# Optimization experiments

Measured on AMD Instinct MI355X. Metric: run time of the kernel, lower is better.

## Reference

```python
import jax, jax.numpy as jnp
import numpy as np

B, N, M = 64, 1024, 1024


def _chamfer(a, b):
    # a: [B,N,3], b: [B,M,3]; pairwise Euclidean distances via Gram trick
    d2 = (
        jnp.sum(a * a, axis=-1)[:, :, None]
        + jnp.sum(b * b, axis=-1)[:, None, :]
        - 2.0 * jnp.einsum('bnd,bmd->bnm', a, b)
    )  # [B,N,M]
    d = jnp.sqrt(jnp.maximum(d2, 0.0))
    # bidirectional nearest-neighbor distance (N == M so they align per-point slot)
    return 0.5 * (jnp.min(d, axis=2) + jnp.min(d, axis=1))  # [B,N]


def _l2(a, b):
    return jnp.linalg.norm(a - b, axis=2)  # [B,N]


def setup_inputs() -> dict:
    key = jax.random.key(0)
    k1, k2, k3, k4, k5, k6 = jax.random.split(key, 6)
    return {
        'pred_points1': jax.random.normal(k1, (B, N, 3), dtype=jnp.float32),
        'pred_points2': jax.random.normal(k2, (B, N, 3), dtype=jnp.float32),
        'target_points': jax.random.normal(k3, (B, M, 3), dtype=jnp.float32),
        'flag1': jax.random.uniform(k4, (B,), dtype=jnp.float32),
        'flag2': jax.random.uniform(k5, (B,), dtype=jnp.float32),
        'sym_flag': jax.random.uniform(k6, (B,), dtype=jnp.float32),
    }


def reference(pred_points1, pred_points2, target_points, flag1, flag2, sym_flag):
    sym_dis1 = _chamfer(pred_points1, target_points).mean(axis=1)   # [B]
    asym_dis1 = _l2(pred_points1, target_points).mean(axis=1)       # [B]
    loss1 = flag1 * (sym_flag * sym_dis1 + (1.0 - sym_flag) * asym_dis1)

    sym_dis2 = _chamfer(pred_points2, target_points).mean(axis=1)
    asym_dis2 = _l2(pred_points2, target_points).mean(axis=1)
    # flag2 multiplier makes the sum(flag2)>0 branch mathematically equivalent
    loss2 = flag2 * (sym_flag * sym_dis2 + (1.0 - sym_flag) * asym_dis2)

    all_loss = loss1 + loss2
    # (all_loss, stage1, stage2) scalar losses, stacked
    return jnp.stack([all_loss.mean(), loss1.mean(), loss2.mean()])
```

## Files before the change

### kernel.cpp

```cpp
#include <hip/hip_runtime.h>
#include <hip/hip_bf16.h>


#define BATCH 64
#define NPTS 1024

typedef __attribute__((ext_vector_type(8))) short s16x8;
typedef __attribute__((ext_vector_type(8))) unsigned short u16x8;
typedef __attribute__((ext_vector_type(16))) float f32x16;

__device__ inline unsigned short f2bf(float v) {
    __hip_bfloat16 h = __float2bfloat16(v);
    return *reinterpret_cast<unsigned short*>(&h);
}
__device__ inline float bf2f(unsigned short u) {
    __hip_bfloat16 h = *reinterpret_cast<__hip_bfloat16*>(&u);
    return __bfloat162float(h);
}

__device__ inline void pack_ab(float x, float y, float z,
                               u16x8& a0, u16x8& a1, u16x8& b0, u16x8& b1) {
    float h = fmaf(z, z, fmaf(y, y, x*x));
    unsigned short xh = f2bf(x), yh = f2bf(y), zh = f2bf(z);
    unsigned short xl = f2bf(x - bf2f(xh)), yl = f2bf(y - bf2f(yh)), zl = f2bf(z - bf2f(zh));
    float cx = -2.f*x, cy = -2.f*y, cz = -2.f*z;
    unsigned short cxh = f2bf(cx), cyh = f2bf(cy), czh = f2bf(cz);
    unsigned short cxl = f2bf(cx - bf2f(cxh)), cyl = f2bf(cy - bf2f(cyh)), czl = f2bf(cz - bf2f(czh));
    unsigned short hh = f2bf(h), hl = f2bf(h - bf2f(hh));
    const unsigned short one = 0x3F80;
    a0 = u16x8{cxh, cyh, czh, cxl, cyl, czl, cxh, cyh};
    a1 = u16x8{czh, hh, hl, one, one, 0, 0, 0};
    b0 = u16x8{xh, yh, zh, xh, yh, zh, xl, yl};
    b1 = u16x8{zl, one, one, hh, hl, 0, 0, 0};
}

__global__ void zero_kernel(float* out) {
    if (threadIdx.x < 3) out[threadIdx.x] = 0.0f;
}

#define TB_OFF   0
#define P1B_OFF  16384
#define P2B_OFF  32768
#define A1_OFF   49152
#define A2_OFF   53248
#define AT_OFF   57344
#define LDS_USH  61440

__device__ inline float fold_sum(float v[16], int lane) {
    {
        const bool up = lane & 1;
        #pragma unroll
        for (int k = 0; k < 8; ++k) {
            float send = up ? v[k] : v[k+8];
            float recv = __shfl_xor(send, 1);
            v[k] = fminf(up ? v[k+8] : v[k], recv);
        }
    }
    {
        const bool up = lane & 2;
        #pragma unroll
        for (int k = 0; k < 4; ++k) {
            float send = up ? v[k] : v[k+4];
            float recv = __shfl_xor(send, 2);
            v[k] = fminf(up ? v[k+4] : v[k], recv);
        }
    }
    {
        const bool up = lane & 4;
        #pragma unroll
        for (int k = 0; k < 2; ++k) {
            float send = up ? v[k] : v[k+2];
            float recv = __shfl_xor(send, 4);
            v[k] = fminf(up ? v[k+2] : v[k], recv);
        }
    }
    {
        const bool up = lane & 8;
        float send = up ? v[0] : v[1];
        float recv = __shfl_xor(send, 8);
        v[0] = fminf(up ? v[1] : v[0], recv);
    }
    v[0] = fminf(v[0], __shfl_xor(v[0], 16));
    float d = sqrtf(fmaxf(v[0], 0.f));
    #pragma unroll
    for (int mask = 1; mask <= 32; mask <<= 1) d += __shfl_xor(d, mask);
    return d;
}

__global__ __launch_bounds__(1024) void chamfer_main(
    const float* __restrict__ p1g, const float* __restrict__ p2g,
    const float* __restrict__ tgg, const float* __restrict__ flag1,
    const float* __restrict__ flag2, const float* __restrict__ symf,
    float* __restrict__ out)
{
    __shared__ __align__(16) unsigned short lds[LDS_USH];
    __shared__ float wsum[16][2];
    __shared__ float esum[16][2];

    const int b = blockIdx.x >> 2, chunk = blockIdx.x & 3;
    const int tid = threadIdx.x;
    const int lane = tid & 63, w = tid >> 6;
    const int c = lane & 31, q = lane >> 5;

    const size_t base = (size_t)b * (NPTS*3) + (size_t)tid * 3;
    const float x1 = p1g[base], y1 = p1g[base+1], z1 = p1g[base+2];
    const float x2 = p2g[base], y2 = p2g[base+1], z2 = p2g[base+2];
    const float xt = tgg[base], yt = tgg[base+1], zt = tgg[base+2];

    const int tile = tid >> 5, r = tid & 31;
    const int bo = tile * 512 + r * 8;
    u16x8 a0, a1, b0, b1;
    pack_ab(x1, y1, z1, a0, a1, b0, b1);
    *(u16x8*)(lds + P1B_OFF + bo)       = b0;
    *(u16x8*)(lds + P1B_OFF + bo + 256) = b1;
    u16x8 A1a0 = a0, A1a1 = a1;
    pack_ab(x2, y2, z2, a0, a1, b0, b1);
    *(u16x8*)(lds + P2B_OFF + bo)       = b0;
    *(u16x8*)(lds + P2B_OFF + bo + 256) = b1;
    u16x8 A2a0 = a0, A2a1 = a1;
    pack_ab(xt, yt, zt, a0, a1, b0, b1);
    *(u16x8*)(lds + TB_OFF + bo)        = b0;
    *(u16x8*)(lds + TB_OFF + bo + 256)  = b1;

    float e1 = 0.f, e2 = 0.f;
    if ((tid >> 8) == chunk) {
        const int j = tid - (chunk << 8);
        const int ao = (j >> 5) * 512 + (j & 31) * 8;
        *(u16x8*)(lds + A1_OFF + ao)       = A1a0;
        *(u16x8*)(lds + A1_OFF + ao + 256) = A1a1;
        *(u16x8*)(lds + A2_OFF + ao)       = A2a0;
        *(u16x8*)(lds + A2_OFF + ao + 256) = A2a1;
        *(u16x8*)(lds + AT_OFF + ao)       = a0;
        *(u16x8*)(lds + AT_OFF + ao + 256) = a1;
        float dx = x1 - xt, dy = y1 - yt, dz = z1 - zt;
        e1 = sqrtf(fmaf(dz, dz, fmaf(dy, dy, dx*dx)));
        dx = x2 - xt; dy = y2 - yt; dz = z2 - zt;
        e2 = sqrtf(fmaf(dz, dz, fmaf(dy, dy, dx*dx)));
    }
    __syncthreads();

    float rm1[16], rm2[16];
    #pragma unroll
    for (int i = 0; i < 16; ++i) { rm1[i] = 3e38f; rm2[i] = 3e38f; }
    const f32x16 zacc = {};
    const int fo = q * 256 + c * 8;

    if (w < 8) {
        const s16x8 fa1 = *(const s16x8*)(lds + A1_OFF + w*512 + fo);
        const s16x8 fa2 = *(const s16x8*)(lds + A2_OFF + w*512 + fo);
        const unsigned short* TBp = lds + TB_OFF + fo;
        #pragma unroll 1
        for (int t = 0; t < 32; t += 2) {
            const s16x8 bb0 = *(const s16x8*)(TBp + t*512);
            const s16x8 bb1 = *(const s16x8*)(TBp + t*512 + 512);
            f32x16 u0 = __builtin_amdgcn_mfma_f32_32x32x16_bf16(fa1, bb0, zacc, 0, 0, 0);
            f32x16 u1 = __builtin_amdgcn_mfma_f32_32x32x16_bf16(fa1, bb1, zacc, 0, 0, 0);
            #pragma unroll
            for (int i = 0; i < 16; ++i) rm1[i] = fminf(fminf(u0[i], u1[i]), rm1[i]);
            u0 = __builtin_amdgcn_mfma_f32_32x32x16_bf16(fa2, bb0, zacc, 0, 0, 0);
            u1 = __builtin_amdgcn_mfma_f32_32x32x16_bf16(fa2, bb1, zacc, 0, 0, 0);
            #pragma unroll
            for (int i = 0; i < 16; ++i) rm2[i] = fminf(fminf(u0[i], u1[i]), rm2[i]);
        }
    } else {
        const s16x8 fat = *(const s16x8*)(lds + AT_OFF + (w-8)*512 + fo);
        const unsigned short* Q1p = lds + P1B_OFF + fo;
        const unsigned short* Q2p = lds + P2B_OFF + fo;
        #pragma unroll 1
        for (int t = 0; t < 32; t += 2) {
            s16x8 bb0 = *(const s16x8*)(Q1p + t*512);
            s16x8 bb1 = *(const s16x8*)(Q1p + t*512 + 512);
            f32x16 u0 = __builtin_amdgcn_mfma_f32_32x32x16_bf16(fat, bb0, zacc, 0, 0, 0);
            f32x16 u1 = __builtin_amdgcn_mfma_f32_32x32x16_bf16(fat, bb1, zacc, 0, 0, 0);
            #pragma unroll
            for (int i = 0; i < 16; ++i) rm1[i] = fminf(fminf(u0[i], u1[i]), rm1[i]);
            bb0 = *(const s16x8*)(Q2p + t*512);
            bb1 = *(const s16x8*)(Q2p + t*512 + 512);
            u0 = __builtin_amdgcn_mfma_f32_32x32x16_bf16(fat, bb0, zacc, 0, 0, 0);
            u1 = __builtin_amdgcn_mfma_f32_32x32x16_bf16(fat, bb1, zacc, 0, 0, 0);
            #pragma unroll
            for (int i = 0; i < 16; ++i) rm2[i] = fminf(fminf(u0[i], u1[i]), rm2[i]);
        }
    }

    const float s1 = fold_sum(rm1, lane);
    const float s2 = fold_sum(rm2, lane);
    #pragma unroll
    for (int mask = 1; mask <= 32; mask <<= 1) {
        e1 += __shfl_xor(e1, mask);
        e2 += __shfl_xor(e2, mask);
    }
    if (lane == 0) {
        wsum[w][0] = s1; wsum[w][1] = s2;
        esum[w][0] = e1; esum[w][1] = e2;
    }
    __syncthreads();

    if (tid == 0) {
        float rowS1 = 0.f, rowS2 = 0.f, colS1 = 0.f, colS2 = 0.f, E1 = 0.f, E2 = 0.f;
        #pragma unroll
        for (int k = 0; k < 8; ++k)  { rowS1 += wsum[k][0]; rowS2 += wsum[k][1]; }
        #pragma unroll
        for (int k = 8; k < 16; ++k) { colS1 += wsum[k][0]; colS2 += wsum[k][1]; }
        #pragma unroll
        for (int k = 0; k < 16; ++k) { E1 += esum[k][0]; E2 += esum[k][1]; }
        const float ch1 = 0.5f * (0.5f * rowS1 + 0.5f * colS1);
        const float ch2 = 0.5f * (0.5f * rowS2 + 0.5f * colS2);
        const float sf = symf[b];
        const float inv = 1.f / (float)NPTS;
        const float l1 = flag1[b] * (sf * ch1 + (1.f - sf) * E1) * inv;
        const float l2 = flag2[b] * (sf * ch2 + (1.f - sf) * E2) * inv;
        const float s = 1.f / (float)BATCH;
        atomicAdd(&out[0], (l1 + l2) * s);
        atomicAdd(&out[1], l1 * s);
        atomicAdd(&out[2], l2 * s);
    }
}

extern "C" void kernel_launch(void* const* d_in, const int* in_sizes, int n_in,
                              void* d_out, int out_size, void* d_ws, size_t ws_size,
                              hipStream_t stream) {
    const float* p1 = (const float*)d_in[0];
    const float* p2 = (const float*)d_in[1];
    const float* tg = (const float*)d_in[2];
    const float* f1 = (const float*)d_in[3];
    const float* f2 = (const float*)d_in[4];
    const float* sf = (const float*)d_in[5];
    float* out = (float*)d_out;

    zero_kernel<<<1, 64, 0, stream>>>(out);
    chamfer_main<<<BATCH * 4, 1024, 0, stream>>>(p1, p2, tg, f1, f2, sf, out);
}
```

Before: 83.82 us.

## Split chamfer into per-direction 512-thread blocks with workspace finalize kernel

Replaces the single 1024-thread block per (batch, quarter) with 1024 smaller 512-thread blocks, one per direction (p1→t, p2→t, t→p1, t→p2) and quarter. Partial sums go to a workspace, and a finalize kernel combines them deterministically instead of zeroing the output and using atomics. The aim is more blocks and a smaller LDS footprint for better occupancy and scheduling. In exchange, each block re-packs the full Y cloud, so packing and global loads are duplicated, and an extra launch dependency is added.

```diff
diff --git a/kernel.cpp b/kernel.cpp
--- a/kernel.cpp
+++ b/kernel.cpp
@@ -34,18 +34,6 @@
     b1 = u16x8{zl, one, one, hh, hl, 0, 0, 0};
 }
 
-__global__ void zero_kernel(float* out) {
-    if (threadIdx.x < 3) out[threadIdx.x] = 0.0f;
-}
-
-#define TB_OFF   0
-#define P1B_OFF  16384
-#define P2B_OFF  32768
-#define A1_OFF   49152
-#define A2_OFF   53248
-#define AT_OFF   57344
-#define LDS_USH  61440
-
 __device__ inline float fold_sum(float v[16], int lane) {
     {
         const bool up = lane & 1;
@@ -87,133 +75,119 @@
     return d;
 }
 
-__global__ __launch_bounds__(1024) void chamfer_main(
-    const float* __restrict__ p1g, const float* __restrict__ p2g,
-    const float* __restrict__ tgg, const float* __restrict__ flag1,
-    const float* __restrict__ flag2, const float* __restrict__ symf,
+__global__ __launch_bounds__(512) void pass_kernel(
+    const float* __restrict__ p1, const float* __restrict__ p2,
+    const float* __restrict__ tg, float* __restrict__ ws)
+{
+    __shared__ __align__(16) unsigned short ybuf[16384];
+    __shared__ __align__(16) unsigned short abuf[4096];
+    __shared__ float red[8];
+    __shared__ float redE[8];
+
+    const int bid = blockIdx.x;
+    const int j = bid >> 8, b = (bid >> 2) & 63, qt = bid & 3;
+    const int tid = threadIdx.x;
+
+    const float* __restrict__ X = (j == 0) ? p1 : (j == 1) ? p2 : tg;
+    const float* __restrict__ Y = (j == 2) ? p1 : (j == 3) ? p2 : tg;
+
+    #pragma unroll
+    for (int ii = 0; ii < 2; ++ii) {
+        const int i = tid + ii * 512;
+        const size_t g = ((size_t)b * NPTS + i) * 3;
+        float x = Y[g], y = Y[g+1], z = Y[g+2];
+        u16x8 a0, a1, b0, b1;
+        pack_ab(x, y, z, a0, a1, b0, b1);
+        const int off = (i >> 5) * 512 + (i & 31) * 8;
+        *(u16x8*)(ybuf + off)       = b0;
+        *(u16x8*)(ybuf + off + 256) = b1;
+    }
+    float e = 0.f;
+    if (tid < 256) {
+        const int i = qt * 256 + tid;
+        const size_t g = ((size_t)b * NPTS + i) * 3;
+        float x = X[g], y = X[g+1], z = X[g+2];
+        u16x8 a0, a1, b0, b1;
+        pack_ab(x, y, z, a0, a1, b0, b1);
+        const int off = (tid >> 5) * 512 + (tid & 31) * 8;
+        *(u16x8*)(abuf + off)       = a0;
+        *(u16x8*)(abuf + off + 256) = a1;
+        if (j < 2) {
+            float tx = tg[g], ty = tg[g+1], tz = tg[g+2];
+            float dx = x - tx, dy = y - ty, dz = z - tz;
+            e = sqrtf(fmaf(dz, dz, fmaf(dy, dy, dx*dx)));
+        }
+    }
+    __syncthreads();
+
+    const int lane = tid & 63, w = tid >> 6;
+    const int c = lane & 31, q = lane >> 5;
+    const int fo = q * 256 + c * 8;
+    const s16x8 fa = *(const s16x8*)(abuf + w * 512 + fo);
+
+    float rm[16];
+    #pragma unroll
+    for (int i = 0; i < 16; ++i) rm[i] = 3e38f;
+    const f32x16 zacc = {};
+
+    const unsigned short* Yp = ybuf + fo;
+    #pragma unroll 1
+    for (int t = 0; t < 32; t += 2) {
+        const s16x8 bb0 = *(const s16x8*)(Yp + t * 512);
+        const s16x8 bb1 = *(const s16x8*)(Yp + t * 512 + 512);
+        f32x16 u0 = __builtin_amdgcn_mfma_f32_32x32x16_bf16(fa, bb0, zacc, 0, 0, 0);
+        f32x16 u1 = __builtin_amdgcn_mfma_f32_32x32x16_bf16(fa, bb1, zacc, 0, 0, 0);
+        #pragma unroll
+        for (int i = 0; i < 16; ++i) rm[i] = fminf(rm[i], fminf(u0[i], u1[i]));
+    }
+
+    const float s = 0.5f * fold_sum(rm, lane);
+    #pragma unroll
+    for (int mask = 1; mask <= 32; mask <<= 1) e += __shfl_xor(e, mask);
+    if (lane == 0) { red[w] = s; redE[w] = e; }
+    __syncthreads();
+
+    if (tid == 0) {
+        float S = 0.f, E = 0.f;
+        #pragma unroll
+        for (int k = 0; k < 8; ++k) { S += red[k]; E += redE[k]; }
+        ws[bid] = S;
+        if (j < 2) ws[1024 + bid] = E;
+    }
+}
+
+__global__ __launch_bounds__(64) void finalize_kernel(
+    const float* __restrict__ flag1, const float* __restrict__ flag2,
+    const float* __restrict__ symf, const float* __restrict__ ws,
     float* __restrict__ out)
 {
-    __shared__ __align__(16) unsigned short lds[LDS_USH];
-    __shared__ float wsum[16][2];
-    __shared__ float esum[16][2];
-
-    const int b = blockIdx.x >> 2, chunk = blockIdx.x & 3;
-    const int tid = threadIdx.x;
-    const int lane = tid & 63, w = tid >> 6;
-    const int c = lane & 31, q = lane >> 5;
-
-    const size_t base = (size_t)b * (NPTS*3) + (size_t)tid * 3;
-    const float x1 = p1g[base], y1 = p1g[base+1], z1 = p1g[base+2];
-    const float x2 = p2g[base], y2 = p2g[base+1], z2 = p2g[base+2];
-    const float xt = tgg[base], yt = tgg[base+1], zt = tgg[base+2];
-
-    const int tile = tid >> 5, r = tid & 31;
-    const int bo = tile * 512 + r * 8;
-    u16x8 a0, a1, b0, b1;
-    pack_ab(x1, y1, z1, a0, a1, b0, b1);
-    *(u16x8*)(lds + P1B_OFF + bo)       = b0;
-    *(u16x8*)(lds + P1B_OFF + bo + 256) = b1;
-    u16x8 A1a0 = a0, A1a1 = a1;
-    pack_ab(x2, y2, z2, a0, a1, b0, b1);
-    *(u16x8*)(lds + P2B_OFF + bo)       = b0;
-    *(u16x8*)(lds + P2B_OFF + bo + 256) = b1;
-    u16x8 A2a0 = a0, A2a1 = a1;
-    pack_ab(xt, yt, zt, a0, a1, b0, b1);
-    *(u16x8*)(lds + TB_OFF + bo)        = b0;
-    *(u16x8*)(lds + TB_OFF + bo + 256)  = b1;
-
-    float e1 = 0.f, e2 = 0.f;
-    if ((tid >> 8) == chunk) {
-        const int j = tid - (chunk << 8);
-        const int ao = (j >> 5) * 512 + (j & 31) * 8;
-        *(u16x8*)(lds + A1_OFF + ao)       = A1a0;
-        *(u16x8*)(lds + A1_OFF + ao + 256) = A1a1;
-        *(u16x8*)(lds + A2_OFF + ao)       = A2a0;
-        *(u16x8*)(lds + A2_OFF + ao + 256) = A2a1;
-        *(u16x8*)(lds + AT_OFF + ao)       = a0;
-        *(u16x8*)(lds + AT_OFF + ao + 256) = a1;
-        float dx = x1 - xt, dy = y1 - yt, dz = z1 - zt;
-        e1 = sqrtf(fmaf(dz, dz, fmaf(dy, dy, dx*dx)));
-        dx = x2 - xt; dy = y2 - yt; dz = z2 - zt;
-        e2 = sqrtf(fmaf(dz, dz, fmaf(dy, dy, dx*dx)));
-    }
-    __syncthreads();
-
-    float rm1[16], rm2[16];
-    #pragma unroll
-    for (int i = 0; i < 16; ++i) { rm1[i] = 3e38f; rm2[i] = 3e38f; }
-    const f32x16 zacc = {};
-    const int fo = q * 256 + c * 8;
-
-    if (w < 8) {
-        const s16x8 fa1 = *(const s16x8*)(lds + A1_OFF + w*512 + fo);
-        const s16x8 fa2 = *(const s16x8*)(lds + A2_OFF + w*512 + fo);
-        const unsigned short* TBp = lds + TB_OFF + fo;
-        #pragma unroll 1
-        for (int t = 0; t < 32; t += 2) {
-            const s16x8 bb0 = *(const s16x8*)(TBp + t*512);
-            const s16x8 bb1 = *(const s16x8*)(TBp + t*512 + 512);
-            f32x16 u0 = __builtin_amdgcn_mfma_f32_32x32x16_bf16(fa1, bb0, zacc, 0, 0, 0);
-            f32x16 u1 = __builtin_amdgcn_mfma_f32_32x32x16_bf16(fa1, bb1, zacc, 0, 0, 0);
-            #pragma unroll
-            for (int i = 0; i < 16; ++i) rm1[i] = fminf(fminf(u0[i], u1[i]), rm1[i]);
-            u0 = __builtin_amdgcn_mfma_f32_32x32x16_bf16(fa2, bb0, zacc, 0, 0, 0);
-            u1 = __builtin_amdgcn_mfma_f32_32x32x16_bf16(fa2, bb1, zacc, 0, 0, 0);
-            #pragma unroll
-            for (int i = 0; i < 16; ++i) rm2[i] = fminf(fminf(u0[i], u1[i]), rm2[i]);
-        }
-    } else {
-        const s16x8 fat = *(const s16x8*)(lds + AT_OFF + (w-8)*512 + fo);
-        const unsigned short* Q1p = lds + P1B_OFF + fo;
-        const unsigned short* Q2p = lds + P2B_OFF + fo;
-        #pragma unroll 1
-        for (int t = 0; t < 32; t += 2) {
-            s16x8 bb0 = *(const s16x8*)(Q1p + t*512);
-            s16x8 bb1 = *(const s16x8*)(Q1p + t*512 + 512);
-            f32x16 u0 = __builtin_amdgcn_mfma_f32_32x32x16_bf16(fat, bb0, zacc, 0, 0, 0);
-            f32x16 u1 = __builtin_amdgcn_mfma_f32_32x32x16_bf16(fat, bb1, zacc, 0, 0, 0);
-            #pragma unroll
-            for (int i = 0; i < 16; ++i) rm1[i] = fminf(fminf(u0[i], u1[i]), rm1[i]);
-            bb0 = *(const s16x8*)(Q2p + t*512);
-            bb1 = *(const s16x8*)(Q2p + t*512 + 512);
-            u0 = __builtin_amdgcn_mfma_f32_32x32x16_bf16(fat, bb0, zacc, 0, 0, 0);
-            u1 = __builtin_amdgcn_mfma_f32_32x32x16_bf16(fat, bb1, zacc, 0, 0, 0);
-            #pragma unroll
-            for (int i = 0; i < 16; ++i) rm2[i] = fminf(fminf(u0[i], u1[i]), rm2[i]);
-        }
-    }
-
-    const float s1 = fold_sum(rm1, lane);
-    const float s2 = fold_sum(rm2, lane);
+    const int b = threadIdx.x;
+    float rowS1 = 0.f, rowS2 = 0.f, colS1 = 0.f, colS2 = 0.f, E1 = 0.f, E2 = 0.f;
+    #pragma unroll
+    for (int qt = 0; qt < 4; ++qt) {
+        rowS1 += ws[0*256 + b*4 + qt];
+        rowS2 += ws[1*256 + b*4 + qt];
+        colS1 += ws[2*256 + b*4 + qt];
+        colS2 += ws[3*256 + b*4 + qt];
+        E1    += ws[1024 + 0*256 + b*4 + qt];
+        E2    += ws[1024 + 1*256 + b*4 + qt];
+    }
+    const float inv = 1.f / (float)NPTS;
+    const float ch1 = 0.5f * (rowS1 + colS1) * inv;
+    const float ch2 = 0.5f * (rowS2 + colS2) * inv;
+    const float sf = symf[b];
+    float l1 = flag1[b] * (sf * ch1 + (1.f - sf) * E1 * inv);
+    float l2 = flag2[b] * (sf * ch2 + (1.f - sf) * E2 * inv);
     #pragma unroll
     for (int mask = 1; mask <= 32; mask <<= 1) {
-        e1 += __shfl_xor(e1, mask);
-        e2 += __shfl_xor(e2, mask);
-    }
-    if (lane == 0) {
-        wsum[w][0] = s1; wsum[w][1] = s2;
-        esum[w][0] = e1; esum[w][1] = e2;
-    }
-    __syncthreads();
-
-    if (tid == 0) {
-        float rowS1 = 0.f, rowS2 = 0.f, colS1 = 0.f, colS2 = 0.f, E1 = 0.f, E2 = 0.f;
-        #pragma unroll
-        for (int k = 0; k < 8; ++k)  { rowS1 += wsum[k][0]; rowS2 += wsum[k][1]; }
-        #pragma unroll
-        for (int k = 8; k < 16; ++k) { colS1 += wsum[k][0]; colS2 += wsum[k][1]; }
-        #pragma unroll
-        for (int k = 0; k < 16; ++k) { E1 += esum[k][0]; E2 += esum[k][1]; }
-        const float ch1 = 0.5f * (0.5f * rowS1 + 0.5f * colS1);
-        const float ch2 = 0.5f * (0.5f * rowS2 + 0.5f * colS2);
-        const float sf = symf[b];
-        const float inv = 1.f / (float)NPTS;
-        const float l1 = flag1[b] * (sf * ch1 + (1.f - sf) * E1) * inv;
-        const float l2 = flag2[b] * (sf * ch2 + (1.f - sf) * E2) * inv;
+        l1 += __shfl_xor(l1, mask);
+        l2 += __shfl_xor(l2, mask);
+    }
+    if (b == 0) {
         const float s = 1.f / (float)BATCH;
-        atomicAdd(&out[0], (l1 + l2) * s);
-        atomicAdd(&out[1], l1 * s);
-        atomicAdd(&out[2], l2 * s);
+        out[0] = (l1 + l2) * s;
+        out[1] = l1 * s;
+        out[2] = l2 * s;
     }
 }
 
@@ -227,7 +201,8 @@
     const float* f2 = (const float*)d_in[4];
     const float* sf = (const float*)d_in[5];
     float* out = (float*)d_out;
-
-    zero_kernel<<<1, 64, 0, stream>>>(out);
-    chamfer_main<<<BATCH * 4, 1024, 0, stream>>>(p1, p2, tg, f1, f2, sf, out);
-}
+    float* ws = (float*)d_ws;
+
+    pass_kernel<<<1024, 512, 0, stream>>>(p1, p2, tg, ws);
+    finalize_kernel<<<1, 64, 0, stream>>>(f1, f2, sf, ws, out);
+}
```

New measurement: 76.21 us. 1.1x faster.
